# Performance work log

Hardware: AMD Instinct MI355X
Metric: run time of the kernel (lower is better)

Reference implementation:

```python
import jax, jax.numpy as jnp
import numpy as np
import math

SCALE = math.sqrt(256.0)

def setup_inputs() -> dict:
    key = jax.random.key(0)
    k1, k2, k3, k4, k5 = jax.random.split(key, 5)
    B, C, T, D = 8, 80, 2048, 256
    bound = 1.0 / math.sqrt(C)
    x = jax.random.normal(k1, (B, C, T), dtype=jnp.float32)
    Wk = jax.random.uniform(k2, (D, C), minval=-bound, maxval=bound, dtype=jnp.float32)
    bk = jax.random.uniform(k3, (D,), minval=-bound, maxval=bound, dtype=jnp.float32)
    Wq = jax.random.uniform(k4, (D, C), minval=-bound, maxval=bound, dtype=jnp.float32)
    bq = jax.random.uniform(k5, (D,), minval=-bound, maxval=bound, dtype=jnp.float32)
    return {"x": x, "Wk": Wk, "bk": bk, "Wq": Wq, "bq": bq}

def reference(x, Wk, bk, Wq, bq):
    # x: [B, C=80, T]; work in time-major layout [B, T, C]
    xt = jnp.swapaxes(x, 1, 2)                      # [B, T, C]
    K = xt @ Wk.T + bk                              # [B, T, 256]
    Q = xt @ Wq.T + bq                              # [B, T, 256]
    # softmax over last dim (dim=2 in torch) of K Q^T / sqrt(256)
    att = jax.nn.softmax(jnp.einsum('bid,bjd->bij', K, Q) / SCALE, axis=2)
    # original per-timestep loop is exactly att @ xt (values = raw input, no V proj)
    out = jnp.einsum('bij,bjc->bic', att, xt)       # [B, T, C]
    return jnp.swapaxes(out, 1, 2)                  # [B, C, T]
```

## Files before the change

### kernel.cpp

```cpp
#include <hip/hip_runtime.h>
#include <hip/hip_bf16.h>
#include <math.h>

typedef __bf16 bf16;
typedef __bf16 bf16x8 __attribute__((ext_vector_type(8)));
typedef float  f32x4  __attribute__((ext_vector_type(4)));
typedef float  f32x16 __attribute__((ext_vector_type(16)));
typedef uint32_t u32x2 __attribute__((ext_vector_type(2)));
typedef uint32_t u32x4 __attribute__((ext_vector_type(4)));

#define MFMA16(a, b, c) __builtin_amdgcn_mfma_f32_16x16x32_bf16((a), (b), (c), 0, 0, 0)
#define MFMA32(a, b, c) __builtin_amdgcn_mfma_f32_32x32x16_bf16((a), (b), (c), 0, 0, 0)

typedef const uint32_t __attribute__((address_space(1)))* gq_t;
typedef uint32_t __attribute__((address_space(3)))* lq_t;

constexpr int B_ = 8, C_ = 80, T_ = 2048, D_ = 256;
constexpr int NS = 4;
constexpr float LOG2E_16 = 0.090169989f;

static __device__ inline uint32_t pkbf(float lo, float hi) {
  bf16 l = (bf16)lo, h = (bf16)hi;
  uint16_t lb = __builtin_bit_cast(uint16_t, l), hb = __builtin_bit_cast(uint16_t, h);
  return (uint32_t)lb | ((uint32_t)hb << 16);
}

constexpr int VF_TILE = 3 * 2 * 2 * 32 * 8;

__global__ __launch_bounds__(256) void wconv_kernel(
    const float* __restrict__ Wk, const float* __restrict__ bk,
    const float* __restrict__ Wq, const float* __restrict__ bq,
    bf16* __restrict__ Wbf)
{
  const int mat = blockIdx.x, d = threadIdx.x;
  const float* W    = mat ? Wq : Wk;
  const float* bias = mat ? bq : bk;
  bf16* row = Wbf + (size_t)(mat * 256 + d) * 96;
  const float bv = bias[d];
  #pragma unroll
  for (int c8 = 0; c8 < 12; ++c8) {
    bf16x8 o;
    #pragma unroll
    for (int e = 0; e < 8; ++e) {
      int c = c8 * 8 + e;
      float v = (c < 80) ? W[d * C_ + c] : (c == 80 ? bv : 0.f);
      o[e] = (bf16)v;
    }
    *reinterpret_cast<bf16x8*>(row + c8 * 8) = o;
  }
}

__global__ __launch_bounds__(256) void proj_kernel(
    const float* __restrict__ x,
    const bf16* __restrict__ Wbf,
    bf16* __restrict__ Kb,
    bf16* __restrict__ Qb,
    bf16* __restrict__ Vf)
{
  const int t0   = blockIdx.x * 32;
  const int b    = blockIdx.y;
  const int tid  = threadIdx.x;
  const int w    = tid >> 6;
  const int lane = tid & 63;
  const int h    = lane >> 4;
  const int lr   = lane & 15;

  const float* xb = x + (size_t)b * C_ * T_;

  {
    bf16* vout = Vf + (size_t)(b * 64 + blockIdx.x) * VF_TILE;
    #pragma unroll
    for (int g = 0; g < 2; ++g) {
      int f = tid + g * 256;
      if (f < 384) {
        int il2 = f & 31, hi2 = (f >> 5) & 1, kj2 = (f >> 6) & 1, cb2 = f >> 7;
        int c = cb2 * 32 + il2;
        bf16x8 o;
        if (c < 80) {
          const float* sp = xb + (size_t)c * T_ + t0 + kj2 * 16 + hi2 * 8;
          f32x4 v0 = *reinterpret_cast<const f32x4*>(sp);
          f32x4 v1 = *reinterpret_cast<const f32x4*>(sp + 4);
          #pragma unroll
          for (int e = 0; e < 4; ++e) { o[e] = (bf16)v0[e]; o[e + 4] = (bf16)v1[e]; }
        } else {
          #pragma unroll
          for (int e = 0; e < 8; ++e) o[e] = (bf16)0.f;
        }
        *reinterpret_cast<bf16x8*>(vout + f * 8) = o;
      }
    }
  }

  bf16x8 afrag[2][3];
  #pragma unroll
  for (int ib = 0; ib < 2; ++ib) {
    int t = t0 + ib * 16 + lr;
    #pragma unroll
    for (int ks = 0; ks < 3; ++ks) {
      bf16x8 v;
      #pragma unroll
      for (int e = 0; e < 8; ++e) {
        int c = ks * 32 + h * 8 + e;
        float val;
        if (c < 80)       val = xb[c * T_ + t];
        else if (c == 80) val = 1.0f;
        else              val = 0.0f;
        v[e] = (bf16)val;
      }
      afrag[ib][ks] = v;
    }
  }

  const int nb0 = w * 4;
  #pragma unroll
  for (int mat = 0; mat < 2; ++mat) {
    bf16* outp = mat ? Qb : Kb;

    f32x4 acc[2][4];
    #pragma unroll
    for (int ib = 0; ib < 2; ++ib)
      #pragma unroll
      for (int nb = 0; nb < 4; ++nb)
        acc[ib][nb] = f32x4{0.f, 0.f, 0.f, 0.f};

    #pragma unroll
    for (int nb = 0; nb < 4; ++nb) {
      int d = (nb0 + nb) * 16 + lr;
      const bf16* wrow = Wbf + (size_t)(mat * 256 + d) * 96;
      #pragma unroll
      for (int ks = 0; ks < 3; ++ks) {
        bf16x8 bv = *reinterpret_cast<const bf16x8*>(wrow + ks * 32 + h * 8);
        #pragma unroll
        for (int ib = 0; ib < 2; ++ib)
          acc[ib][nb] = MFMA16(afrag[ib][ks], bv, acc[ib][nb]);
      }
    }

    #pragma unroll
    for (int ib = 0; ib < 2; ++ib)
      #pragma unroll
      for (int nb = 0; nb < 4; ++nb) {
        int d = (nb0 + nb) * 16 + lr;
        #pragma unroll
        for (int r = 0; r < 4; ++r) {
          int t = t0 + ib * 16 + h * 4 + r;
          outp[(size_t)(b * T_ + t) * D_ + d] = (bf16)acc[ib][nb][r];
        }
      }
  }
}

__global__ __launch_bounds__(256, 2) void attn_kernel(
    const bf16* __restrict__ Kb,
    const bf16* __restrict__ Qb,
    const bf16* __restrict__ Vf,
    float* __restrict__ Opart,
    float* __restrict__ mpart,
    float* __restrict__ lpart)
{
  constexpr int BN = 64, NSTG = T_ / BN;
  constexpr int STG_PER = NSTG / NS;
  __shared__ bf16 qlds[2][BN * D_];

  const int flat = blockIdx.x;
  const int b    = flat & 7;
  const int rem  = flat >> 3;
  const int it   = rem & 15;
  const int s    = rem >> 4;
  const int i0   = it * 128;

  const int tid  = threadIdx.x;
  const int w    = tid >> 6;
  const int lane = tid & 63;
  const int il   = lane & 31;
  const int hi   = lane >> 5;
  const int iw   = i0 + w * 32;

  const bf16* Kbase = Kb + (size_t)b * T_ * D_;
  const bf16* Qbase = Qb + (size_t)b * T_ * D_;
  const bf16* Vbase = Vf + (size_t)b * 64 * VF_TILE;

  bf16x8 kf[16];
  {
    const bf16* kp = Kbase + (size_t)(iw + il) * D_ + hi * 8;
    #pragma unroll
    for (int ks = 0; ks < 16; ++ks)
      kf[ks] = *reinterpret_cast<const bf16x8*>(kp + ks * 16);
  }

  f32x16 oacc[3];
  #pragma unroll
  for (int cb = 0; cb < 3; ++cb)
    #pragma unroll
    for (int r = 0; r < 16; ++r) oacc[cb][r] = 0.f;
  float m_run = -INFINITY, l_run = 0.f;

  const int st0 = s * STG_PER;
  const int off = (it & 3) * 2;
  auto smap = [&](int t) { return st0 + ((t - st0 + off) & (STG_PER - 1)); };

  auto stage = [&](int st, int buf) {
    #pragma unroll
    for (int q = 0; q < 8; ++q) {
      int f = tid + 256 * q;
      int j = f >> 5, c = f & 31;
      const bf16* src = Qbase + (size_t)(st * BN + j) * D_ + ((c ^ (j & 31)) << 3);
      __builtin_amdgcn_global_load_lds((gq_t)src,
          (lq_t)&qlds[buf][(q * 256 + w * 64) * 8], 16, 0, 0);
    }
  };

  auto qkt = [&](int buf, int hf, f32x16& sc) {
    #pragma unroll
    for (int r = 0; r < 16; ++r) sc[r] = 0.f;
    __builtin_amdgcn_s_setprio(1);
    #pragma unroll
    for (int ks = 0; ks < 16; ++ks) {
      bf16x8 qa = *reinterpret_cast<const bf16x8*>(
          &qlds[buf][(hf * 32 + il) * 256 + (((hi + 2 * ks) ^ il) << 3)]);
      sc = MFMA32(qa, kf[ks], sc);
    }
    __builtin_amdgcn_s_setprio(0);
  };

  auto smax_pv = [&](f32x16& sacc, bf16x8 (&vf)[3][2]) {
    float p16[16];
    #pragma unroll
    for (int r = 0; r < 16; ++r) p16[r] = sacc[r];
    float q0 = fmaxf(fmaxf(p16[0],  p16[1]),  p16[2]);
    float q1 = fmaxf(fmaxf(p16[3],  p16[4]),  p16[5]);
    float q2 = fmaxf(fmaxf(p16[6],  p16[7]),  p16[8]);
    float q3 = fmaxf(fmaxf(p16[9],  p16[10]), p16[11]);
    float q4 = fmaxf(fmaxf(p16[12], p16[13]), p16[14]);
    float mx = fmaxf(fmaxf(fmaxf(q0, q1), q2),
                     fmaxf(fmaxf(q3, q4), p16[15]));
    mx = fmaxf(mx, __shfl_xor(mx, 32));

    if (!__all(mx <= m_run + 48.f)) {
      float mnew  = fmaxf(m_run, mx);
      float alpha = exp2f((m_run - mnew) * LOG2E_16);
      m_run = mnew;
      l_run *= alpha;
      #pragma unroll
      for (int cb = 0; cb < 3; ++cb)
        #pragma unroll
        for (int r = 0; r < 16; ++r) oacc[cb][r] *= alpha;
    }
    #pragma unroll
    for (int r = 0; r < 16; ++r)
      p16[r] = exp2f((p16[r] - m_run) * LOG2E_16);
    {
      float s0 = (p16[0] + p16[1]) + (p16[2] + p16[3]);
      float s1 = (p16[4] + p16[5]) + (p16[6] + p16[7]);
      float s2 = (p16[8] + p16[9]) + (p16[10] + p16[11]);
      float s3 = (p16[12] + p16[13]) + (p16[14] + p16[15]);
      l_run += (s0 + s1) + (s2 + s3);
    }

    uint32_t a0 = pkbf(p16[0],  p16[1]),  a1 = pkbf(p16[2],  p16[3]);
    uint32_t c0 = pkbf(p16[4],  p16[5]),  c1 = pkbf(p16[6],  p16[7]);
    uint32_t a2 = pkbf(p16[8],  p16[9]),  a3 = pkbf(p16[10], p16[11]);
    uint32_t c2 = pkbf(p16[12], p16[13]), c3 = pkbf(p16[14], p16[15]);
    u32x2 w0 = __builtin_amdgcn_permlane32_swap(a0, c0, false, false);
    u32x2 w1 = __builtin_amdgcn_permlane32_swap(a1, c1, false, false);
    u32x2 w2 = __builtin_amdgcn_permlane32_swap(a2, c2, false, false);
    u32x2 w3 = __builtin_amdgcn_permlane32_swap(a3, c3, false, false);
    u32x4 pb0 = { w0[0], w1[0], w0[1], w1[1] };
    u32x4 pb1 = { w2[0], w3[0], w2[1], w3[1] };
    bf16x8 pbf0 = __builtin_bit_cast(bf16x8, pb0);
    bf16x8 pbf1 = __builtin_bit_cast(bf16x8, pb1);

    __builtin_amdgcn_s_setprio(1);
    #pragma unroll
    for (int cb = 0; cb < 3; ++cb) {
      oacc[cb] = MFMA32(vf[cb][0], pbf0, oacc[cb]);
      oacc[cb] = MFMA32(vf[cb][1], pbf1, oacc[cb]);
    }
    __builtin_amdgcn_s_setprio(0);
  };

  auto vload = [&](int j32, bf16x8 (&vf)[3][2]) {
    const bf16* vt = Vbase + (size_t)j32 * VF_TILE + lane * 8;
    #pragma unroll
    for (int cb = 0; cb < 3; ++cb)
      #pragma unroll
      for (int kj = 0; kj < 2; ++kj)
        vf[cb][kj] = *reinterpret_cast<const bf16x8*>(vt + (cb * 2 + kj) * 512);
  };

  stage(smap(st0), 0);
  asm volatile("s_waitcnt vmcnt(0)" ::: "memory");
  __syncthreads();

  int cur = 0;
  for (int t = st0; t < st0 + STG_PER; ++t, cur ^= 1) {
    const int st = smap(t);
    if (t + 1 < st0 + STG_PER) stage(smap(t + 1), cur ^ 1);

    bf16x8 vf0[3][2], vf1[3][2];
    vload(st * 2, vf0);

    f32x16 sacc0, sacc1;
    qkt(cur, 0, sacc0);
    qkt(cur, 1, sacc1);

    smax_pv(sacc0, vf0);
    vload(st * 2 + 1, vf1);
    smax_pv(sacc1, vf1);

    asm volatile("s_waitcnt vmcnt(0)" ::: "memory");
    __syncthreads();
  }

  l_run += __shfl_xor(l_run, 32);

  float* ob = Opart + (size_t)(s * B_ + b) * C_ * T_;
  #pragma unroll
  for (int cb = 0; cb < 3; ++cb)
    #pragma unroll
    for (int r = 0; r < 16; ++r) {
      if (cb < 2 || r < 8) {
        int c = cb * 32 + (r & 3) + 8 * (r >> 2) + 4 * hi;
        ob[(size_t)c * T_ + iw + il] = oacc[cb][r];
      }
    }
  if (lane < 32) {
    mpart[(size_t)(s * B_ + b) * T_ + iw + il] = m_run;
    lpart[(size_t)(s * B_ + b) * T_ + iw + il] = l_run;
  }
}

__global__ __launch_bounds__(256) void merge_kernel(
    const float* __restrict__ Opart,
    const float* __restrict__ mpart,
    const float* __restrict__ lpart,
    float* __restrict__ out)
{
  const int b    = blockIdx.y;
  const int tid  = threadIdx.x;
  const int slot = tid & 3;
  const int c1   = tid >> 2;
  const int t4   = blockIdx.x * 16 + slot * 4;

  f32x4 m[NS], e[NS];
  f32x4 mmax;
  #pragma unroll
  for (int s2 = 0; s2 < NS; ++s2)
    m[s2] = *reinterpret_cast<const f32x4*>(&mpart[(size_t)(s2 * B_ + b) * T_ + t4]);
  #pragma unroll
  for (int r = 0; r < 4; ++r) {
    mmax[r] = m[0][r];
    #pragma unroll
    for (int s2 = 1; s2 < NS; ++s2) mmax[r] = fmaxf(mmax[r], m[s2][r]);
  }
  f32x4 lsum = f32x4{0.f, 0.f, 0.f, 0.f};
  #pragma unroll
  for (int s2 = 0; s2 < NS; ++s2) {
    f32x4 lv = *reinterpret_cast<const f32x4*>(&lpart[(size_t)(s2 * B_ + b) * T_ + t4]);
    #pragma unroll
    for (int r = 0; r < 4; ++r) e[s2][r] = exp2f((m[s2][r] - mmax[r]) * LOG2E_16);
    lsum += e[s2] * lv;
  }
  f32x4 inv;
  #pragma unroll
  for (int r = 0; r < 4; ++r) inv[r] = 1.0f / lsum[r];

  #pragma unroll
  for (int pass = 0; pass < 2; ++pass) {
    const int c = c1 + pass * 64;
    if (pass == 0 || c1 < 16) {
      f32x4 acc = f32x4{0.f, 0.f, 0.f, 0.f};
      #pragma unroll
      for (int s2 = 0; s2 < NS; ++s2)
        acc += *reinterpret_cast<const f32x4*>(
                   &Opart[((size_t)(s2 * B_ + b) * C_ + c) * T_ + t4]) * e[s2];
      *reinterpret_cast<f32x4*>(&out[((size_t)b * C_ + c) * T_ + t4]) = acc * inv;
    }
  }
}

extern "C" void kernel_launch(void* const* d_in, const int* in_sizes, int n_in,
                              void* d_out, int out_size, void* d_ws, size_t ws_size,
                              hipStream_t stream) {
  (void)in_sizes; (void)n_in; (void)out_size; (void)ws_size;
  const float* x  = (const float*)d_in[0];
  const float* Wk = (const float*)d_in[1];
  const float* bk = (const float*)d_in[2];
  const float* Wq = (const float*)d_in[3];
  const float* bq = (const float*)d_in[4];
  float* out = (float*)d_out;

  char* ws = (char*)d_ws;
  const size_t MB = 1024 * 1024;
  bf16*  Kb    = (bf16*)(ws);
  bf16*  Qb    = (bf16*)(ws + 8 * MB);
  bf16*  Vf    = (bf16*)(ws + 16 * MB);
  bf16*  Wbf   = (bf16*)(ws + 19 * MB);
  float* Opart = (float*)(ws + 20 * MB);
  float* mpart = (float*)(ws + 42 * MB);
  float* lpart = (float*)(ws + 43 * MB);

  dim3 blk(256);
  wconv_kernel<<<dim3(2), blk, 0, stream>>>(Wk, bk, Wq, bq, Wbf);
  dim3 g1(T_ / 32, B_);
  proj_kernel<<<g1, blk, 0, stream>>>(x, Wbf, Kb, Qb, Vf);
  attn_kernel<<<dim3(16 * NS * B_), blk, 0, stream>>>(Kb, Qb, Vf, Opart, mpart, lpart);
  dim3 g3(T_ / 16, B_);
  merge_kernel<<<g3, blk, 0, stream>>>(Opart, mpart, lpart, out);
}
```

Measured before the change: 68.76 us.

## Stage x tile in LDS for projection, widen weight-convert grid, serialize attention halves

The projection kernel now loads the 80x32 x tile once into shared memory with vectorized loads and builds both the V fragments and the A fragments from LDS, replacing strided scalar global reads. The weight conversion kernel is split over 24 blocks instead of 2 so each thread writes one 8-element chunk. In the attention loop the two 32-row halves are processed one after another (V load, QK^T, softmax, PV per half) instead of computing both score tiles first, which lowers register pressure but reduces overlap between the two halves.

```diff
diff --git a/kernel.cpp b/kernel.cpp
--- a/kernel.cpp
+++ b/kernel.cpp
@@ -32,22 +32,17 @@
     const float* __restrict__ Wq, const float* __restrict__ bq,
     bf16* __restrict__ Wbf)
 {
-  const int mat = blockIdx.x, d = threadIdx.x;
+  const int mat = blockIdx.x, c8 = blockIdx.y, d = threadIdx.x;
   const float* W    = mat ? Wq : Wk;
   const float* bias = mat ? bq : bk;
-  bf16* row = Wbf + (size_t)(mat * 256 + d) * 96;
-  const float bv = bias[d];
-  #pragma unroll
-  for (int c8 = 0; c8 < 12; ++c8) {
-    bf16x8 o;
-    #pragma unroll
-    for (int e = 0; e < 8; ++e) {
-      int c = c8 * 8 + e;
-      float v = (c < 80) ? W[d * C_ + c] : (c == 80 ? bv : 0.f);
-      o[e] = (bf16)v;
-    }
-    *reinterpret_cast<bf16x8*>(row + c8 * 8) = o;
-  }
+  bf16x8 o;
+  #pragma unroll
+  for (int e = 0; e < 8; ++e) {
+    int c = c8 * 8 + e;
+    float v = (c < 80) ? W[d * C_ + c] : (c == 80 ? bias[d] : 0.f);
+    o[e] = (bf16)v;
+  }
+  *reinterpret_cast<bf16x8*>(Wbf + (size_t)(mat * 256 + d) * 96 + c8 * 8) = o;
 }
 
 __global__ __launch_bounds__(256) void proj_kernel(
@@ -57,6 +52,8 @@
     bf16* __restrict__ Qb,
     bf16* __restrict__ Vf)
 {
+  __shared__ float xlds[80 * 36];
+
   const int t0   = blockIdx.x * 32;
   const int b    = blockIdx.y;
   const int tid  = threadIdx.x;
@@ -67,6 +64,17 @@
 
   const float* xb = x + (size_t)b * C_ * T_;
 
+  #pragma unroll
+  for (int q = 0; q < 3; ++q) {
+    int id = tid + q * 256;
+    if (id < 640) {
+      int c = id >> 3, ch = id & 7;
+      f32x4 v = *reinterpret_cast<const f32x4*>(xb + (size_t)c * T_ + t0 + ch * 4);
+      *reinterpret_cast<f32x4*>(&xlds[c * 36 + ch * 4]) = v;
+    }
+  }
+  __syncthreads();
+
   {
     bf16* vout = Vf + (size_t)(b * 64 + blockIdx.x) * VF_TILE;
     #pragma unroll
@@ -77,7 +85,7 @@
         int c = cb2 * 32 + il2;
         bf16x8 o;
         if (c < 80) {
-          const float* sp = xb + (size_t)c * T_ + t0 + kj2 * 16 + hi2 * 8;
+          const float* sp = &xlds[c * 36 + kj2 * 16 + hi2 * 8];
           f32x4 v0 = *reinterpret_cast<const f32x4*>(sp);
           f32x4 v1 = *reinterpret_cast<const f32x4*>(sp + 4);
           #pragma unroll
@@ -94,7 +102,6 @@
   bf16x8 afrag[2][3];
   #pragma unroll
   for (int ib = 0; ib < 2; ++ib) {
-    int t = t0 + ib * 16 + lr;
     #pragma unroll
     for (int ks = 0; ks < 3; ++ks) {
       bf16x8 v;
@@ -102,7 +109,7 @@
       for (int e = 0; e < 8; ++e) {
         int c = ks * 32 + h * 8 + e;
         float val;
-        if (c < 80)       val = xb[c * T_ + t];
+        if (c < 80)       val = xlds[c * 36 + ib * 16 + lr];
         else if (c == 80) val = 1.0f;
         else              val = 0.0f;
         v[e] = (bf16)val;
@@ -210,84 +217,6 @@
     }
   };
 
-  auto qkt = [&](int buf, int hf, f32x16& sc) {
-    #pragma unroll
-    for (int r = 0; r < 16; ++r) sc[r] = 0.f;
-    __builtin_amdgcn_s_setprio(1);
-    #pragma unroll
-    for (int ks = 0; ks < 16; ++ks) {
-      bf16x8 qa = *reinterpret_cast<const bf16x8*>(
-          &qlds[buf][(hf * 32 + il) * 256 + (((hi + 2 * ks) ^ il) << 3)]);
-      sc = MFMA32(qa, kf[ks], sc);
-    }
-    __builtin_amdgcn_s_setprio(0);
-  };
-
-  auto smax_pv = [&](f32x16& sacc, bf16x8 (&vf)[3][2]) {
-    float p16[16];
-    #pragma unroll
-    for (int r = 0; r < 16; ++r) p16[r] = sacc[r];
-    float q0 = fmaxf(fmaxf(p16[0],  p16[1]),  p16[2]);
-    float q1 = fmaxf(fmaxf(p16[3],  p16[4]),  p16[5]);
-    float q2 = fmaxf(fmaxf(p16[6],  p16[7]),  p16[8]);
-    float q3 = fmaxf(fmaxf(p16[9],  p16[10]), p16[11]);
-    float q4 = fmaxf(fmaxf(p16[12], p16[13]), p16[14]);
-    float mx = fmaxf(fmaxf(fmaxf(q0, q1), q2),
-                     fmaxf(fmaxf(q3, q4), p16[15]));
-    mx = fmaxf(mx, __shfl_xor(mx, 32));
-
-    if (!__all(mx <= m_run + 48.f)) {
-      float mnew  = fmaxf(m_run, mx);
-      float alpha = exp2f((m_run - mnew) * LOG2E_16);
-      m_run = mnew;
-      l_run *= alpha;
-      #pragma unroll
-      for (int cb = 0; cb < 3; ++cb)
-        #pragma unroll
-        for (int r = 0; r < 16; ++r) oacc[cb][r] *= alpha;
-    }
-    #pragma unroll
-    for (int r = 0; r < 16; ++r)
-      p16[r] = exp2f((p16[r] - m_run) * LOG2E_16);
-    {
-      float s0 = (p16[0] + p16[1]) + (p16[2] + p16[3]);
-      float s1 = (p16[4] + p16[5]) + (p16[6] + p16[7]);
-      float s2 = (p16[8] + p16[9]) + (p16[10] + p16[11]);
-      float s3 = (p16[12] + p16[13]) + (p16[14] + p16[15]);
-      l_run += (s0 + s1) + (s2 + s3);
-    }
-
-    uint32_t a0 = pkbf(p16[0],  p16[1]),  a1 = pkbf(p16[2],  p16[3]);
-    uint32_t c0 = pkbf(p16[4],  p16[5]),  c1 = pkbf(p16[6],  p16[7]);
-    uint32_t a2 = pkbf(p16[8],  p16[9]),  a3 = pkbf(p16[10], p16[11]);
-    uint32_t c2 = pkbf(p16[12], p16[13]), c3 = pkbf(p16[14], p16[15]);
-    u32x2 w0 = __builtin_amdgcn_permlane32_swap(a0, c0, false, false);
-    u32x2 w1 = __builtin_amdgcn_permlane32_swap(a1, c1, false, false);
-    u32x2 w2 = __builtin_amdgcn_permlane32_swap(a2, c2, false, false);
-    u32x2 w3 = __builtin_amdgcn_permlane32_swap(a3, c3, false, false);
-    u32x4 pb0 = { w0[0], w1[0], w0[1], w1[1] };
-    u32x4 pb1 = { w2[0], w3[0], w2[1], w3[1] };
-    bf16x8 pbf0 = __builtin_bit_cast(bf16x8, pb0);
-    bf16x8 pbf1 = __builtin_bit_cast(bf16x8, pb1);
-
-    __builtin_amdgcn_s_setprio(1);
-    #pragma unroll
-    for (int cb = 0; cb < 3; ++cb) {
-      oacc[cb] = MFMA32(vf[cb][0], pbf0, oacc[cb]);
-      oacc[cb] = MFMA32(vf[cb][1], pbf1, oacc[cb]);
-    }
-    __builtin_amdgcn_s_setprio(0);
-  };
-
-  auto vload = [&](int j32, bf16x8 (&vf)[3][2]) {
-    const bf16* vt = Vbase + (size_t)j32 * VF_TILE + lane * 8;
-    #pragma unroll
-    for (int cb = 0; cb < 3; ++cb)
-      #pragma unroll
-      for (int kj = 0; kj < 2; ++kj)
-        vf[cb][kj] = *reinterpret_cast<const bf16x8*>(vt + (cb * 2 + kj) * 512);
-  };
-
   stage(smap(st0), 0);
   asm volatile("s_waitcnt vmcnt(0)" ::: "memory");
   __syncthreads();
@@ -297,16 +226,84 @@
     const int st = smap(t);
     if (t + 1 < st0 + STG_PER) stage(smap(t + 1), cur ^ 1);
 
-    bf16x8 vf0[3][2], vf1[3][2];
-    vload(st * 2, vf0);
-
-    f32x16 sacc0, sacc1;
-    qkt(cur, 0, sacc0);
-    qkt(cur, 1, sacc1);
-
-    smax_pv(sacc0, vf0);
-    vload(st * 2 + 1, vf1);
-    smax_pv(sacc1, vf1);
+    #pragma unroll
+    for (int hf = 0; hf < 2; ++hf) {
+      const int j32 = st * 2 + hf;
+
+      const bf16* vt = Vbase + (size_t)j32 * VF_TILE + lane * 8;
+      bf16x8 vf[3][2];
+      #pragma unroll
+      for (int cb = 0; cb < 3; ++cb)
+        #pragma unroll
+        for (int kj = 0; kj < 2; ++kj)
+          vf[cb][kj] = *reinterpret_cast<const bf16x8*>(vt + (cb * 2 + kj) * 512);
+
+      f32x16 sacc;
+      #pragma unroll
+      for (int r = 0; r < 16; ++r) sacc[r] = 0.f;
+      __builtin_amdgcn_s_setprio(1);
+      #pragma unroll
+      for (int ks = 0; ks < 16; ++ks) {
+        bf16x8 qa = *reinterpret_cast<const bf16x8*>(
+            &qlds[cur][(hf * 32 + il) * 256 + (((hi + 2 * ks) ^ il) << 3)]);
+        sacc = MFMA32(qa, kf[ks], sacc);
+      }
+      __builtin_amdgcn_s_setprio(0);
+
+      float p16[16];
+      #pragma unroll
+      for (int r = 0; r < 16; ++r) p16[r] = sacc[r];
+      float q0 = fmaxf(fmaxf(p16[0],  p16[1]),  p16[2]);
+      float q1 = fmaxf(fmaxf(p16[3],  p16[4]),  p16[5]);
+      float q2 = fmaxf(fmaxf(p16[6],  p16[7]),  p16[8]);
+      float q3 = fmaxf(fmaxf(p16[9],  p16[10]), p16[11]);
+      float q4 = fmaxf(fmaxf(p16[12], p16[13]), p16[14]);
+      float mx = fmaxf(fmaxf(fmaxf(q0, q1), q2),
+                       fmaxf(fmaxf(q3, q4), p16[15]));
+      mx = fmaxf(mx, __shfl_xor(mx, 32));
+
+      if (!__all(mx <= m_run + 48.f)) {
+        float mnew  = fmaxf(m_run, mx);
+        float alpha = exp2f((m_run - mnew) * LOG2E_16);
+        m_run = mnew;
+        l_run *= alpha;
+        #pragma unroll
+        for (int cb = 0; cb < 3; ++cb)
+          #pragma unroll
+          for (int r = 0; r < 16; ++r) oacc[cb][r] *= alpha;
+      }
+      #pragma unroll
+      for (int r = 0; r < 16; ++r)
+        p16[r] = exp2f((p16[r] - m_run) * LOG2E_16);
+      {
+        float s0 = (p16[0] + p16[1]) + (p16[2] + p16[3]);
+        float s1 = (p16[4] + p16[5]) + (p16[6] + p16[7]);
+        float s2 = (p16[8] + p16[9]) + (p16[10] + p16[11]);
+        float s3 = (p16[12] + p16[13]) + (p16[14] + p16[15]);
+        l_run += (s0 + s1) + (s2 + s3);
+      }
+
+      uint32_t a0 = pkbf(p16[0],  p16[1]),  a1 = pkbf(p16[2],  p16[3]);
+      uint32_t c0 = pkbf(p16[4],  p16[5]),  c1 = pkbf(p16[6],  p16[7]);
+      uint32_t a2 = pkbf(p16[8],  p16[9]),  a3 = pkbf(p16[10], p16[11]);
+      uint32_t c2 = pkbf(p16[12], p16[13]), c3 = pkbf(p16[14], p16[15]);
+      u32x2 w0 = __builtin_amdgcn_permlane32_swap(a0, c0, false, false);
+      u32x2 w1 = __builtin_amdgcn_permlane32_swap(a1, c1, false, false);
+      u32x2 w2 = __builtin_amdgcn_permlane32_swap(a2, c2, false, false);
+      u32x2 w3 = __builtin_amdgcn_permlane32_swap(a3, c3, false, false);
+      u32x4 pb0 = { w0[0], w1[0], w0[1], w1[1] };
+      u32x4 pb1 = { w2[0], w3[0], w2[1], w3[1] };
+      bf16x8 pbf0 = __builtin_bit_cast(bf16x8, pb0);
+      bf16x8 pbf1 = __builtin_bit_cast(bf16x8, pb1);
+
+      __builtin_amdgcn_s_setprio(1);
+      #pragma unroll
+      for (int cb = 0; cb < 3; ++cb) {
+        oacc[cb] = MFMA32(vf[cb][0], pbf0, oacc[cb]);
+        oacc[cb] = MFMA32(vf[cb][1], pbf1, oacc[cb]);
+      }
+      __builtin_amdgcn_s_setprio(0);
+    }
 
     asm volatile("s_waitcnt vmcnt(0)" ::: "memory");
     __syncthreads();
@@ -401,7 +398,7 @@
   float* lpart = (float*)(ws + 43 * MB);
 
   dim3 blk(256);
-  wconv_kernel<<<dim3(2), blk, 0, stream>>>(Wk, bk, Wq, bq, Wbf);
+  wconv_kernel<<<dim3(2, 12), blk, 0, stream>>>(Wk, bk, Wq, bq, Wbf);
   dim3 g1(T_ / 32, B_);
   proj_kernel<<<g1, blk, 0, stream>>>(x, Wbf, Kb, Qb, Vf);
   attn_kernel<<<dim3(16 * NS * B_), blk, 0, stream>>>(Kb, Qb, Vf, Opart, mpart, lpart);
```

Measured after the change: 66.16 us. -3.8%, faster.
